# Performance work log

Measured on AMD Instinct MI355X. Metric: run time of the kernel, lower is better.

The kernel has to match this reference:

```python
import jax, jax.numpy as jnp
import numpy as np

# ---- static config (matches init_kwargs) ----
B, N, DIM = 1, 2048, 1024
H, KVH, D = 16, 8, 64
GQ = H // KVH                 # grouped queries per kv head
WS = 64                       # sliding window size (causal, exact)
CBS, STRIDE = 32, 16          # compress block size / sliding stride
SEL_BLK, NSEL, NMEM = 32, 4, 1
NCB = N // STRIDE             # num compressed blocks (128)
NFB = N // SEL_BLK            # num fine blocks (64)
NCPF = SEL_BLK // STRIDE      # compressed blocks per fine block (2)
HID = CBS * D                 # compress MLP hidden (expand factor 1.0)
SCALE = D ** -0.5
THETA = 10000.0
NEG = -jnp.finfo(jnp.float32).max


def setup_inputs():
    key = jax.random.key(0)
    ks = jax.random.split(key, 16)
    s = 0.02
    r = lambda i, shape: jax.random.normal(ks[i], shape, jnp.float32) * s
    return {
        "inp": jax.random.normal(ks[0], (B, N, DIM), jnp.float32),
        "norm_g": jnp.ones((DIM,), jnp.float32),
        "Wqkv": r(1, (DIM, (H + 2 * KVH) * D)),
        "mem_kv": r(2, (2, KVH, NMEM, D)),
        "k_pos": r(3, (KVH, CBS, D)),
        "v_pos": r(4, (KVH, CBS, D)),
        "kW1": r(5, (CBS * D, HID)), "kb1": jnp.zeros((HID,), jnp.float32),
        "kW2": r(6, (HID, D)), "kb2": jnp.zeros((D,), jnp.float32),
        "vW1": r(7, (CBS * D, HID)), "vb1": jnp.zeros((HID,), jnp.float32),
        "vW2": r(8, (HID, D)), "vb2": jnp.zeros((D,), jnp.float32),
        "combW": r(9, (DIM, 3 * H)),
        "combB": jnp.tile(jnp.array([-2.0, -2.0, 2.0], jnp.float32), H),
        "Wout": r(10, (H * D, DIM)),
    }


def _rope(t):
    # lucidrains rotary-embedding-torch: interleaved adjacent-pair rotation
    inv_freq = 1.0 / (THETA ** (jnp.arange(0, D, 2, dtype=jnp.float32) / D))
    ang = jnp.arange(N, dtype=jnp.float32)[:, None] * inv_freq        # [N, D/2]
    cos = jnp.repeat(jnp.cos(ang), 2, axis=-1)                        # [N, D]
    sin = jnp.repeat(jnp.sin(ang), 2, axis=-1)
    t2 = t.reshape(*t.shape[:-1], D // 2, 2)
    rot = jnp.stack([-t2[..., 1], t2[..., 0]], axis=-1).reshape(t.shape)
    return t * cos + rot * sin


def _forward(inp, norm_g, Wqkv, mem_kv, k_pos, v_pos,
             kW1, kb1, kW2, kb2, vW1, vb1, vW2, vb2,
             combW, combB, Wout):
    # RMSNorm
    x = inp * jax.lax.rsqrt(jnp.mean(inp * inp, -1, keepdims=True)
                            + jnp.finfo(inp.dtype).eps) * norm_g
    qkv = x @ Wqkv
    q, k, v = jnp.split(qkv, [H * D, H * D + KVH * D], axis=-1)
    q = q.reshape(B, N, H, D).transpose(0, 2, 1, 3)      # b h n d
    k = k.reshape(B, N, KVH, D).transpose(0, 2, 1, 3)    # b kvh n d
    v = v.reshape(B, N, KVH, D).transpose(0, 2, 1, 3)

    # ---- compressed branch (overlapping windows, left zero pad) ----
    overlap = CBS - STRIDE
    kp = jnp.pad(k, ((0, 0), (0, 0), (overlap, 0), (0, 0)))
    vp = jnp.pad(v, ((0, 0), (0, 0), (overlap, 0), (0, 0)))
    widx = jnp.arange(NCB)[:, None] * STRIDE + jnp.arange(CBS)[None, :]  # [NCB, CBS]
    kw = kp[:, :, widx] + k_pos[None, :, None]   # b kvh w cbs d
    vw = vp[:, :, widx] + v_pos[None, :, None]

    def cmlp(t, W1, b1, W2, b2):
        t = t.reshape(B, KVH, NCB, CBS * D)
        return jax.nn.relu(t @ W1 + b1) @ W2 + b2       # b kvh w d

    ck = cmlp(kw, kW1, kb1, kW2, kb2)
    cv = cmlp(vw, vW1, vb1, vW2, vb2)
    ck = jnp.concatenate([jnp.broadcast_to(mem_kv[0], (B, KVH, NMEM, D)), ck], 2)
    cv = jnp.concatenate([jnp.broadcast_to(mem_kv[1], (B, KVH, NMEM, D)), cv], 2)

    qg = q.reshape(B, KVH, GQ, N, D)
    csim = jnp.einsum('bhgid,bhjd->bhgij', qg, ck) * SCALE   # no mask (cmask=None)
    cattn = jax.nn.softmax(csim, -1)
    cout = jnp.einsum('bhgij,bhjd->bhgid', cattn, cv).reshape(B, H, N, D)

    # rotary AFTER compressed attention (as in source)
    rq, rk = _rope(q), _rope(k)

    # ---- importance scores -> top-k fine block selection ----
    imp = csim[..., NMEM:].mean(2)                          # b kvh n NCB (share grouped q)
    imp = imp.reshape(B, KVH, N, NFB, NCPF).mean(-1)        # mean-pool to fine blocks
    q_blk = jnp.arange(N) // SEL_BLK
    diag = q_blk[:, None] == jnp.arange(NFB)[None, :]
    imp = jnp.where(diag[None, None], NEG, imp)             # mask own (diagonal) block
    imp = jax.nn.softmax(jnp.pad(imp, ((0, 0),) * 3 + ((1, 0),),
                                 constant_values=-1000.0), -1)[..., 1:]
    sel_val, sel_idx = jax.lax.top_k(imp, NSEL)             # b kvh n NSEL

    # ---- fine (block-selected) attention ----
    own = jnp.broadcast_to(q_blk[None, None, :, None], (B, KVH, N, 1))
    sel_idx = jnp.concatenate([sel_idx, own], -1)           # append own block
    fmask = jnp.repeat((sel_val > 1e-10)[..., None], SEL_BLK, -1)  # b kvh n NSEL blk
    causal_row = jnp.tril(jnp.ones((SEL_BLK, SEL_BLK), bool))[jnp.arange(N) % SEL_BLK]
    causal = jnp.broadcast_to(causal_row[None, None, :, None, :],
                              (B, KVH, N, 1, SEL_BLK))
    fmask = jnp.concatenate([fmask, causal], 3).reshape(B, KVH, N, (NSEL + 1) * SEL_BLK)

    fk_blocks = rk.reshape(B, KVH, NFB, SEL_BLK, D)
    fv_blocks = v.reshape(B, KVH, NFB, SEL_BLK, D)
    gather = jax.vmap(jax.vmap(lambda blocks, idx: blocks[idx]))  # over b, kvh
    fk = gather(fk_blocks, sel_idx).reshape(B, KVH, N, (NSEL + 1) * SEL_BLK, D)
    fv = gather(fv_blocks, sel_idx).reshape(B, KVH, N, (NSEL + 1) * SEL_BLK, D)

    rqg = rq.reshape(B, KVH, GQ, N, D)
    fsim = jnp.einsum('bhgid,bhijd->bhgij', rqg, fk) * SCALE
    fsim = jnp.where(fmask[:, :, None], fsim, NEG / 10)
    fattn = jax.nn.softmax(fsim, -1)
    fout = jnp.einsum('bhgij,bhijd->bhgid', fattn, fv).reshape(B, H, N, D)

    # ---- sliding window (causal, exact window size WS) ----
    NW = N // WS
    kp2 = jnp.pad(rk, ((0, 0), (0, 0), (WS, 0), (0, 0)))
    vp2 = jnp.pad(v, ((0, 0), (0, 0), (WS, 0), (0, 0)))
    kidx = jnp.arange(NW)[:, None] * WS + jnp.arange(2 * WS)[None, :]
    kwin = kp2[:, :, kidx]                                  # b kvh nw 2ws d
    vwin = vp2[:, :, kidx]
    qwin = rqg.reshape(B, KVH, GQ, NW, WS, D)
    ssim = jnp.einsum('bhgwid,bhwjd->bhgwij', qwin, kwin) * SCALE
    i = jnp.arange(WS)[:, None]
    j = jnp.arange(2 * WS)[None, :]
    diff = i - (j - WS)
    local_ok = (diff >= 0) & (diff < WS)                    # [WS, 2WS]
    keypos = jnp.arange(NW)[:, None, None] * WS + (jnp.arange(2 * WS) - WS)[None, None, :]
    smask = local_ok[None] & (keypos >= 0)                  # [NW, WS, 2WS]
    ssim = jnp.where(smask[None, None, None], ssim, NEG)
    sattn = jax.nn.softmax(ssim, -1)
    sout = jnp.einsum('bhgwij,bhwjd->bhgwid', sattn, vwin).reshape(B, H, N, D)

    # ---- learned strategy combination (compressed, fine, sliding) ----
    gates = jax.nn.sigmoid(x @ combW + combB).reshape(B, N, H, 3).transpose(0, 2, 1, 3)
    out = gates[..., 0:1] * cout + gates[..., 1:2] * fout + gates[..., 2:3] * sout
    out = out.transpose(0, 2, 1, 3).reshape(B, N, H * D) @ Wout
    return out


def reference(inp, norm_g, Wqkv, mem_kv, k_pos, v_pos,
              kW1, kb1, kW2, kb2, vW1, vb1, vW2, vb2,
              combW, combB, Wout):
    return _forward(inp, norm_g, Wqkv, mem_kv, k_pos, v_pos,
                    kW1, kb1, kW2, kb2, vW1, vb1, vW2, vb2,
                    combW, combB, Wout)
```

## Files before the change

kernel.cpp:

```cpp
#include <hip/hip_runtime.h>
#include <hip/hip_bf16.h>

#define NTOK 2048
#define DIM 1024
#define NH 16
#define KVH 8
#define GQ 2
#define HD 64
#define WS 64
#define CBS 32
#define STRIDE 16
#define SEL_BLK 32
#define NSEL 4
#define NMEM 1
#define NCB 128
#define NFB 64
#define HIDN 2048
#define SCALE 0.125f
#define NEGF (-3.4028234663852886e38f)
#define NEG10F (-3.4028234663852886e37f)

typedef __attribute__((ext_vector_type(8))) short bf16x8;
typedef __attribute__((ext_vector_type(4))) float f32x4;

__device__ __forceinline__ float bflo(unsigned u) { return __uint_as_float(u << 16); }
__device__ __forceinline__ float bfhi(unsigned u) { return __uint_as_float(u & 0xffff0000u); }
__device__ __forceinline__ void dot8(const float4& qa, const float4& qb, uint4 a, float& s) {
    s += qa.x * bflo(a.x) + qa.y * bfhi(a.x) + qa.z * bflo(a.y) + qa.w * bfhi(a.y) +
         qb.x * bflo(a.z) + qb.y * bfhi(a.z) + qb.z * bflo(a.w) + qb.w * bfhi(a.w);
}

__device__ __forceinline__ void gload_lds16(const void* g, void* l) {
    __builtin_amdgcn_global_load_lds((const __attribute__((address_space(1))) unsigned*)g,
                                     (__attribute__((address_space(3))) unsigned*)l, 16, 0, 0);
}

__global__ __launch_bounds__(256) void rmsnorm_kernel(const float* __restrict__ inp,
                                                      const float* __restrict__ g,
                                                      float* __restrict__ x,
                                                      __hip_bfloat16* __restrict__ xb) {
    int n = blockIdx.x;
    const float* row = inp + (size_t)n * DIM;
    float ss = 0.f;
    for (int c = threadIdx.x; c < DIM; c += 256) { float v = row[c]; ss += v * v; }
    __shared__ float red[4];
    for (int o = 32; o; o >>= 1) ss += __shfl_down(ss, o, 64);
    if ((threadIdx.x & 63) == 0) red[threadIdx.x >> 6] = ss;
    __syncthreads();
    if (threadIdx.x == 0) red[0] = red[0] + red[1] + red[2] + red[3];
    __syncthreads();
    float rs = 1.0f / sqrtf(red[0] / (float)DIM + 1.1920928955078125e-07f);
    float* xr = x + (size_t)n * DIM;
    __hip_bfloat16* xbr = xb + (size_t)n * DIM;
    for (int c = threadIdx.x; c < DIM; c += 256) {
        float v = row[c] * rs * g[c];
        xr[c] = v;
        xbr[c] = __float2bfloat16(v);
    }
}

__device__ __forceinline__ void transpose_body(const float* __restrict__ B,
                                               __hip_bfloat16* __restrict__ Bt,
                                               int K, int N, int bx, int by) {
    __shared__ float tile[32][33];
    int n0 = bx * 32, k0 = by * 32;
    int x = threadIdx.x & 31, y = threadIdx.x >> 5;
    for (int i = 0; i < 4; i++) {
        int k = k0 + y + 8 * i, n = n0 + x;
        tile[y + 8 * i][x] = (k < K && n < N) ? B[(size_t)k * N + n] : 0.f;
    }
    __syncthreads();
    for (int i = 0; i < 4; i++) {
        int n = n0 + y + 8 * i, k = k0 + x;
        if (n < N && k < K) Bt[(size_t)n * K + k] = __float2bfloat16(tile[x][y + 8 * i]);
    }
}

__global__ __launch_bounds__(256) void transpose_all_kernel(
    const float* Wqkv, __hip_bfloat16* Wqkvt,
    const float* kW1, __hip_bfloat16* kW1t,
    const float* vW1, __hip_bfloat16* vW1t,
    const float* Wout, __hip_bfloat16* Woutt,
    const float* combW, __hip_bfloat16* combWt,
    const float* kW2, __hip_bfloat16* kW2t,
    const float* vW2, __hip_bfloat16* vW2t) {
    int b = blockIdx.x;
    if (b < 2048) { transpose_body(Wqkv, Wqkvt, 1024, 2048, b % 64, b / 64); return; }
    b -= 2048;
    if (b < 4096) { transpose_body(kW1, kW1t, 2048, 2048, b % 64, b / 64); return; }
    b -= 4096;
    if (b < 4096) { transpose_body(vW1, vW1t, 2048, 2048, b % 64, b / 64); return; }
    b -= 4096;
    if (b < 1024) { transpose_body(Wout, Woutt, 1024, 1024, b % 32, b / 32); return; }
    b -= 1024;
    if (b < 64) { transpose_body(combW, combWt, 1024, 48, b % 2, b / 2); return; }
    b -= 64;
    if (b < 128) { transpose_body(kW2, kW2t, 2048, 64, b % 2, b / 2); return; }
    b -= 128;
    transpose_body(vW2, vW2t, 2048, 64, b % 2, b / 2);
}

template <int ACT, int OUTBF16>
__device__ __forceinline__ void mfma_gemm_body(const __hip_bfloat16* __restrict__ A,
                                               const __hip_bfloat16* __restrict__ Bt,
                                               const float* __restrict__ bias,
                                               void* __restrict__ Cp,
                                               int M, int N, int K, int bx, int by) {
    __shared__ __align__(16) short As[128 * 32];
    __shared__ __align__(16) short Bs[128 * 32];
    int tid = threadIdx.x;
    int lane = tid & 63, wave = tid >> 6;
    int wm = (wave >> 1) * 64, wn = (wave & 1) * 64;
    int m0 = by * 128, n0 = bx * 128;
    f32x4 acc[4][4];
    for (int r = 0; r < 4; r++)
        for (int c = 0; c < 4; c++)
            acc[r][c] = (f32x4){0.f, 0.f, 0.f, 0.f};

    int r0 = tid >> 2, kc0 = (tid & 3) * 8;
    int r1 = r0 + 64;

    for (int k0 = 0; k0 < K; k0 += 32) {
        __syncthreads();
        gload_lds16(A + (size_t)(m0 + r0) * K + k0 + kc0, &As[r0 * 32 + kc0]);
        gload_lds16(A + (size_t)(m0 + r1) * K + k0 + kc0, &As[r1 * 32 + kc0]);
        gload_lds16(Bt + (size_t)(n0 + r0) * K + k0 + kc0, &Bs[r0 * 32 + kc0]);
        gload_lds16(Bt + (size_t)(n0 + r1) * K + k0 + kc0, &Bs[r1 * 32 + kc0]);
        __syncthreads();
        bf16x8 af[4], bfr[4];
#pragma unroll
        for (int r = 0; r < 4; r++)
            af[r] = *(const bf16x8*)&As[(wm + r * 16 + (lane & 15)) * 32 + (lane >> 4) * 8];
#pragma unroll
// ... 19 lines not shown
                else
                    ((float*)Cp)[(size_t)(grow + v) * N + gcol] = val;
            }
        }
    }
}

template <int ACT, int OUTBF16>
__global__ __launch_bounds__(256) void mfma_gemm(const __hip_bfloat16* __restrict__ A,
                                                 const __hip_bfloat16* __restrict__ Bt,
                                                 const float* __restrict__ bias,
                                                 void* __restrict__ Cp,
                                                 int M, int N, int K) {
    mfma_gemm_body<ACT, OUTBF16>(A, Bt, bias, Cp, M, N, K, blockIdx.x, blockIdx.y);
}

__global__ __launch_bounds__(256) void mfma_gemm_pair(const __hip_bfloat16* A0,
                                                      const __hip_bfloat16* A1,
                                                      const __hip_bfloat16* Bt0,
                                                      const __hip_bfloat16* Bt1,
                                                      const float* bias0, const float* bias1,
                                                      __hip_bfloat16* C0, __hip_bfloat16* C1,
                                                      int M, int N, int K) {
    if (blockIdx.z == 0)
        mfma_gemm_body<1, 1>(A0, Bt0, bias0, C0, M, N, K, blockIdx.x, blockIdx.y);
    else
        mfma_gemm_body<1, 1>(A1, Bt1, bias1, C1, M, N, K, blockIdx.x, blockIdx.y);
}

__device__ __forceinline__ void skgemm_body(const __hip_bfloat16* __restrict__ A,
                                            const __hip_bfloat16* __restrict__ Bt,
                                            float* __restrict__ C,
                                            int M, int Nout, int K, int by, int bz, int nz) {
    __shared__ __align__(16) short As[128 * 32];
    __shared__ __align__(16) short Bs[64 * 32];
    int tid = threadIdx.x;
    int lane = tid & 63, wave = tid >> 6;
    int m0 = by * 128;
    int wm = wave * 32;
    int kchunk = K / nz;
    int kbase = bz * kchunk;
    f32x4 acc[2][4];
    for (int r = 0; r < 2; r++)
        for (int c = 0; c < 4; c++) acc[r][c] = (f32x4){0.f, 0.f, 0.f, 0.f};

    int ra = tid >> 2, kc = (tid & 3) * 8;
    int rb = ra < Nout ? ra : Nout - 1;
    for (int k0 = kbase; k0 < kbase + kchunk; k0 += 32) {
        __syncthreads();
        gload_lds16(A + (size_t)(m0 + ra) * K + k0 + kc, &As[ra * 32 + kc]);
        gload_lds16(A + (size_t)(m0 + ra + 64) * K + k0 + kc, &As[(ra + 64) * 32 + kc]);
        gload_lds16(Bt + (size_t)rb * K + k0 + kc, &Bs[ra * 32 + kc]);
        __syncthreads();
        bf16x8 af[2], bfr[4];
#pragma unroll
        for (int r = 0; r < 2; r++)
            af[r] = *(const bf16x8*)&As[(wm + r * 16 + (lane & 15)) * 32 + (lane >> 4) * 8];
#pragma unroll
        for (int c = 0; c < 4; c++)
            bfr[c] = *(const bf16x8*)&Bs[(c * 16 + (lane & 15)) * 32 + (lane >> 4) * 8];
#pragma unroll
        for (int r = 0; r < 2; r++)
#pragma unroll
            for (int c = 0; c < 4; c++)
                acc[r][c] = __builtin_amdgcn_mfma_f32_16x16x32_bf16(af[r], bfr[c], acc[r][c], 0, 0, 0);
    }
    for (int r = 0; r < 2; r++) {
        int grow = m0 + wm + r * 16 + (lane >> 4) * 4;
        for (int c = 0; c < 4; c++) {
            int gcol = c * 16 + (lane & 15);
            if (gcol >= Nout) continue;
#pragma unroll
            for (int v = 0; v < 4; v++)
                atomicAdd(&C[(size_t)(grow + v) * Nout + gcol], acc[r][c][v]);
        }
    }
}

__global__ __launch_bounds__(256) void skgemm_kernel(const __hip_bfloat16* __restrict__ A,
                                                     const __hip_bfloat16* __restrict__ Bt,
                                                     float* __restrict__ C,
                                                     int M, int Nout, int K) {
    skgemm_body(A, Bt, C, M, Nout, K, blockIdx.y, blockIdx.z, gridDim.z);
}

__global__ __launch_bounds__(256) void skgemm_pair(const __hip_bfloat16* A0,
                                                   const __hip_bfloat16* A1,
                                                   const __hip_bfloat16* Bt0,
                                                   const __hip_bfloat16* Bt1,
                                                   float* C0, float* C1,
                                                   int M, int Nout, int K) {
    if (blockIdx.x == 0)
        skgemm_body(A0, Bt0, C0, M, Nout, K, blockIdx.y, blockIdx.z, gridDim.z);
    else
        skgemm_body(A1, Bt1, C1, M, Nout, K, blockIdx.y, blockIdx.z, gridDim.z);
}

__global__ __launch_bounds__(256) void initbias2_kernel(float* __restrict__ C0,
                                                        const float* __restrict__ b0,
                                                        float* __restrict__ C1,
                                                        const float* __restrict__ b1,
                                                        int M, int Nout) {
    int idx = blockIdx.x * 256 + threadIdx.x;
    int tot = M * Nout;
    if (idx < tot) C0[idx] = b0[idx % Nout];
    else if (idx < 2 * tot) { idx -= tot; C1[idx] = b1[idx % Nout]; }
}

__global__ __launch_bounds__(256) void initbias_kernel(float* __restrict__ C,
                                                       const float* __restrict__ bias,
                                                       int M, int Nout) {
    int idx = blockIdx.x * 256 + threadIdx.x;
    if (idx < M * Nout) C[idx] = bias[idx % Nout];
}

__global__ __launch_bounds__(256) void buildwin_kernel(const float* __restrict__ qkv,
                                                       const float* __restrict__ k_pos,
                                                       const float* __restrict__ v_pos,
                                                       __hip_bfloat16* __restrict__ kwflat,
                                                       __hip_bfloat16* __restrict__ vwflat) {
    size_t total = (size_t)(KVH * NCB) * HIDN;
    for (size_t e = (size_t)blockIdx.x * 256 + threadIdx.x; e < total;
         e += (size_t)gridDim.x * 256) {
        int r = (int)(e >> 11);
        int c = (int)(e & 2047);
        int j = c >> 6, d = c & 63;
        int h = r >> 7, i = r & 127;
        int p = i * STRIDE + j - (CBS - STRIDE);
        float kb = k_pos[((size_t)h * CBS + j) * HD + d];
        float vb = v_pos[((size_t)h * CBS + j) * HD + d];
        float kv = 0.f, vv = 0.f;
        if (p >= 0) {
            kv = qkv[(size_t)p * 2048 + 1024 + h * HD + d];
            vv = qkv[(size_t)p * 2048 + 1536 + h * HD + d];
        }
        kwflat[e] = __float2bfloat16(kv + kb);
        vwflat[e] = __float2bfloat16(vv + vb);
    }
}

__global__ __launch_bounds__(256) void rope_kernel(const float* __restrict__ qkv,
                                                   float* __restrict__ rq,
                                                   __hip_bfloat16* __restrict__ rk,
                                                   __hip_bfloat16* __restrict__ vt) {
    int n = blockIdx.x;
    int t = threadIdx.x;
    for (int idx = t; idx < NH * 32; idx += 256) {
        int h = idx >> 5, f = idx & 31;
        float inv = exp2f((float)f * -0.41524101186092f);
        float ang = (float)n * inv;
        float cc = cosf(ang), ssn = sinf(ang);
        float a = qkv[(size_t)n * 2048 + h * HD + 2 * f];
        float b = qkv[(size_t)n * 2048 + h * HD + 2 * f + 1];
        float* o = rq + ((size_t)h * NTOK + n) * HD + 2 * f;
        o[0] = a * cc - b * ssn;
        o[1] = b * cc + a * ssn;
    }
    for (int idx = t; idx < KVH * 32; idx += 256) {
        int h = idx >> 5, f = idx & 31;
        float inv = exp2f((float)f * -0.41524101186092f);
        float ang = (float)n * inv;
        float cc = cosf(ang), ssn = sinf(ang);
        float a = qkv[(size_t)n * 2048 + 1024 + h * HD + 2 * f];
        float b = qkv[(size_t)n * 2048 + 1024 + h * HD + 2 * f + 1];
        __hip_bfloat16* o = rk + ((size_t)h * NTOK + n) * HD + 2 * f;
        o[0] = __float2bfloat16(a * cc - b * ssn);
        o[1] = __float2bfloat16(b * cc + a * ssn);
    }
    for (int idx = t; idx < KVH * HD; idx += 256) {
        int h = idx >> 6, d = idx & 63;
        vt[((size_t)h * NTOK + n) * HD + d] =
            __float2bfloat16(qkv[(size_t)n * 2048 + 1536 + h * HD + d]);
    }
}

__global__ __launch_bounds__(256) void cattn2_kernel(const float* __restrict__ qkv,
                                                     const float* __restrict__ ckraw,
                                                     const float* __restrict__ cvraw,
                                                     const float* __restrict__ memkv,
                                                     float* __restrict__ cout,
                                                     int* __restrict__ selidx,
                                                     int* __restrict__ selmask) {
    int h = blockIdx.x >> 6;
    int i0 = (blockIdx.x & 63) * 32;
    int t = threadIdx.x;
    __shared__ float qs[64][68];
    __shared__ float sc[64][132];
    __shared__ float scratch[32 * 68];
    __shared__ float memk[64], memv[64];

    for (int idx = t; idx < 4096; idx += 256) {
        int row = idx >> 6, d = idx & 63;
        int g = row >> 5, qi = row & 31;
        qs[row][d] = qkv[(size_t)(i0 + qi) * 2048 + (h * 2 + g) * 64 + d];
    }
    if (t < 64) { memk[t] = memkv[h * 64 + t]; memv[t] = memkv[(8 + h) * 64 + t]; }
    __syncthreads();
    if (t < 64) {
        float s = 0.f;
        for (int d = 0; d < 64; d++) s += qs[t][d] * memk[d];
// ... 76 lines not shown
            o1[dd] = p1 * v;
        }
    }
    for (int c = 0; c < 4; c++) {
        __syncthreads();
        for (int idx = t; idx < 2048; idx += 256) {
            int jj = idx >> 6, d = idx & 63;
            scratch[jj * 68 + d] = cvraw[((size_t)h * 128 + c * 32 + jj) * 64 + d];
        }
        __syncthreads();
        for (int jj = 0; jj < 32; jj++) {
            float p0 = sc[rg * 2][1 + c * 32 + jj];
            float p1 = sc[rg * 2 + 1][1 + c * 32 + jj];
#pragma unroll
            for (int dd = 0; dd < 8; dd++) {
                float v = scratch[jj * 68 + dg + dd * 8];
                o0[dd] += p0 * v;
                o1[dd] += p1 * v;
            }
        }
    }
    {
        int row = rg * 2;
        int g = row >> 5, qi = row & 31;
        int g2 = (row + 1) >> 5, qi2 = (row + 1) & 31;
#pragma unroll
        for (int dd = 0; dd < 8; dd++) {
            cout[(((size_t)(h * 2 + g)) * NTOK + i0 + qi) * 64 + dd * 8 + dg] = o0[dd];
            cout[(((size_t)(h * 2 + g2)) * NTOK + i0 + qi2) * 64 + dd * 8 + dg] = o1[dd];
        }
    }
}

__global__ __launch_bounds__(256) void attn_fused_kernel(const float* __restrict__ rq,
                                                         const __hip_bfloat16* __restrict__ rk,
                                                         const __hip_bfloat16* __restrict__ vt,
                                                         const int* __restrict__ selidx,
                                                         const int* __restrict__ selmask,
                                                         float* __restrict__ fout,
                                                         float* __restrict__ sout) {
    int ws = threadIdx.x >> 6, lane = threadIdx.x & 63;
    __shared__ float sp[4][2][160];
    __shared__ int sel[4][5];
    __shared__ int smk[4];
    float* p0 = sp[ws][0];
    float* p1 = sp[ws][1];

    int kq = lane >> 2, c = lane & 3;
    int kv8 = lane >> 3, c8 = lane & 7;

    if (blockIdx.x < 4096) {
        int wid = blockIdx.x * 4 + ws;
        int h = wid >> 11, i = wid & 2047;
        if (lane < 5) sel[ws][lane] = selidx[((size_t)h * NTOK + i) * 5 + lane];
        if (lane == 5) smk[ws] = selmask[h * NTOK + i];

        const float* q0p = rq + ((size_t)(h * 2 + 0) * NTOK + i) * 64 + c * 16;
        const float* q1p = rq + ((size_t)(h * 2 + 1) * NTOK + i) * 64 + c * 16;
        float4 q0[4], q1[4];
#pragma unroll
        for (int u = 0; u < 4; u++) {
            q0[u] = *(const float4*)(q0p + u * 4);
            q1[u] = *(const float4*)(q1p + u * 4);
        }
        __syncthreads();
        int mk = smk[ws];
        int iq = i & 31;
#pragma unroll
        for (int kt = 0; kt < 10; kt++) {
            int slot = kt >> 1;
            int blk = sel[ws][slot];
            int key = kt * 16 + kq;
            int jj = key & 31;
            int kpos = blk * 32 + jj;
            bool valid = (slot < 4) ? (((mk >> slot) & 1) != 0) : (jj <= iq);
            const __hip_bfloat16* kr = rk + ((size_t)h * NTOK + kpos) * 64 + c * 16;
            float s0 = 0.f, s1 = 0.f;
            uint4 a = *(const uint4*)(kr);
            uint4 b = *(const uint4*)(kr + 8);
            dot8(q0[0], q0[1], a, s0); dot8(q0[2], q0[3], b, s0);
            dot8(q1[0], q1[1], a, s1); dot8(q1[2], q1[3], b, s1);
            s0 += __shfl_xor(s0, 1); s0 += __shfl_xor(s0, 2);
            s1 += __shfl_xor(s1, 1); s1 += __shfl_xor(s1, 2);
            if (c == 0) {
                p0[key] = valid ? s0 * SCALE : NEG10F;
// ... 33 lines not shown
        for (int slot = 0; slot < 5; slot++) {
            const __hip_bfloat16* vbase = vt + ((size_t)h * NTOK + sel[ws][slot] * 32) * 64;
#pragma unroll
            for (int pass = 0; pass < 4; pass++) {
                int j = pass * 8 + kv8;
                uint4 v = *(const uint4*)(vbase + j * 64 + c8 * 8);
                float pa = p0[slot * 32 + j], pb = p1[slot * 32 + j];
                float e0 = bflo(v.x), e1 = bfhi(v.x), e2 = bflo(v.y), e3 = bfhi(v.y);
                float e4 = bflo(v.z), e5 = bfhi(v.z), e6 = bflo(v.w), e7 = bfhi(v.w);
                o0[0] = fmaf(pa, e0, o0[0]); o0[1] = fmaf(pa, e1, o0[1]);
                o0[2] = fmaf(pa, e2, o0[2]); o0[3] = fmaf(pa, e3, o0[3]);
                o0[4] = fmaf(pa, e4, o0[4]); o0[5] = fmaf(pa, e5, o0[5]);
                o0[6] = fmaf(pa, e6, o0[6]); o0[7] = fmaf(pa, e7, o0[7]);
                o1[0] = fmaf(pb, e0, o1[0]); o1[1] = fmaf(pb, e1, o1[1]);
                o1[2] = fmaf(pb, e2, o1[2]); o1[3] = fmaf(pb, e3, o1[3]);
                o1[4] = fmaf(pb, e4, o1[4]); o1[5] = fmaf(pb, e5, o1[5]);
                o1[6] = fmaf(pb, e6, o1[6]); o1[7] = fmaf(pb, e7, o1[7]);
            }
        }
#pragma unroll
        for (int o = 8; o <= 32; o <<= 1)
#pragma unroll
            for (int d = 0; d < 8; d++) {
                o0[d] += __shfl_xor(o0[d], o);
                o1[d] += __shfl_xor(o1[d], o);
            }
        if (kv8 == 0) {
            float* f0 = fout + ((size_t)(h * 2 + 0) * NTOK + i) * 64 + c8 * 8;
            float* f1 = fout + ((size_t)(h * 2 + 1) * NTOK + i) * 64 + c8 * 8;
            *(float4*)(f0) = (float4){o0[0], o0[1], o0[2], o0[3]};
            *(float4*)(f0 + 4) = (float4){o0[4], o0[5], o0[6], o0[7]};
            *(float4*)(f1) = (float4){o1[0], o1[1], o1[2], o1[3]};
            *(float4*)(f1 + 4) = (float4){o1[4], o1[5], o1[6], o1[7]};
        }
    } else {
        int wid = (blockIdx.x - 4096) * 4 + ws;
        int h = wid >> 11, i = wid & 2047;
        const float* q0p = rq + ((size_t)(h * 2 + 0) * NTOK + i) * 64 + c * 16;
        const float* q1p = rq + ((size_t)(h * 2 + 1) * NTOK + i) * 64 + c * 16;
        float4 q0[4], q1[4];
#pragma unroll
        for (int u = 0; u < 4; u++) {
            q0[u] = *(const float4*)(q0p + u * 4);
            q1[u] = *(const float4*)(q1p + u * 4);
        }
#pragma unroll
        for (int kt = 0; kt < 4; kt++) {
            int key = kt * 16 + kq;
            int kpos = i - 63 + key;
            int kp = kpos < 0 ? 0 : kpos;
            const __hip_bfloat16* kr = rk + ((size_t)h * NTOK + kp) * 64 + c * 16;
            float s0 = 0.f, s1 = 0.f;
            uint4 a = *(const uint4*)(kr);
            uint4 b = *(const uint4*)(kr + 8);
            dot8(q0[0], q0[1], a, s0); dot8(q0[2], q0[3], b, s0);
            dot8(q1[0], q1[1], a, s1); dot8(q1[2], q1[3], b, s1);
            s0 += __shfl_xor(s0, 1); s0 += __shfl_xor(s0, 2);
            s1 += __shfl_xor(s1, 1); s1 += __shfl_xor(s1, 2);
            if (c == 0) {
                p0[key] = (kpos >= 0) ? s0 * SCALE : NEG10F;
                p1[key] = (kpos >= 0) ? s1 * SCALE : NEG10F;
            }
        }
        __syncthreads();
        {
            float a0 = p0[lane], a1 = p1[lane];
            float m0 = a0, m1 = a1;
#pragma unroll
            for (int o = 1; o < 64; o <<= 1) {
                m0 = fmaxf(m0, __shfl_xor(m0, o));
                m1 = fmaxf(m1, __shfl_xor(m1, o));
            }
            float e0 = __expf(a0 - m0), e1 = __expf(a1 - m1);
            float d0 = e0, d1 = e1;
#pragma unroll
            for (int o = 1; o < 64; o <<= 1) {
                d0 += __shfl_xor(d0, o);
                d1 += __shfl_xor(d1, o);
            }
            p0[lane] = e0 / d0;
            p1[lane] = e1 / d1;
        }
        __syncthreads();
        int base = i - 63;
        float o0[8] = {}, o1[8] = {};
        const __hip_bfloat16* vbase = vt + (size_t)h * NTOK * 64;
#pragma unroll
        for (int pass = 0; pass < 8; pass++) {
            int j = pass * 8 + kv8;
            int kpos = base + j;
            int kp = kpos < 0 ? 0 : kpos;
            uint4 v = *(const uint4*)(vbase + (size_t)kp * 64 + c8 * 8);
            float pa = p0[j], pb = p1[j];
            float e0 = bflo(v.x), e1 = bfhi(v.x), e2 = bflo(v.y), e3 = bfhi(v.y);
            float e4 = bflo(v.z), e5 = bfhi(v.z), e6 = bflo(v.w), e7 = bfhi(v.w);
            o0[0] = fmaf(pa, e0, o0[0]); o0[1] = fmaf(pa, e1, o0[1]);
            o0[2] = fmaf(pa, e2, o0[2]); o0[3] = fmaf(pa, e3, o0[3]);
            o0[4] = fmaf(pa, e4, o0[4]); o0[5] = fmaf(pa, e5, o0[5]);
            o0[6] = fmaf(pa, e6, o0[6]); o0[7] = fmaf(pa, e7, o0[7]);
            o1[0] = fmaf(pb, e0, o1[0]); o1[1] = fmaf(pb, e1, o1[1]);
            o1[2] = fmaf(pb, e2, o1[2]); o1[3] = fmaf(pb, e3, o1[3]);
            o1[4] = fmaf(pb, e4, o1[4]); o1[5] = fmaf(pb, e5, o1[5]);
            o1[6] = fmaf(pb, e6, o1[6]); o1[7] = fmaf(pb, e7, o1[7]);
        }
#pragma unroll
        for (int o = 8; o <= 32; o <<= 1)
#pragma unroll
            for (int d = 0; d < 8; d++) {
                o0[d] += __shfl_xor(o0[d], o);
                o1[d] += __shfl_xor(o1[d], o);
            }
        if (kv8 == 0) {
            float* s0p = sout + ((size_t)(h * 2 + 0) * NTOK + i) * 64 + c8 * 8;
            float* s1p = sout + ((size_t)(h * 2 + 1) * NTOK + i) * 64 + c8 * 8;
            *(float4*)(s0p) = (float4){o0[0], o0[1], o0[2], o0[3]};
            *(float4*)(s0p + 4) = (float4){o0[4], o0[5], o0[6], o0[7]};
            *(float4*)(s1p) = (float4){o1[0], o1[1], o1[2], o1[3]};
            *(float4*)(s1p + 4) = (float4){o1[4], o1[5], o1[6], o1[7]};
        }
    }
}

__global__ __launch_bounds__(256) void combine_kernel(const float* __restrict__ gateslin,
                                                      const float* __restrict__ cout,
                                                      const float* __restrict__ fout,
                                                      const float* __restrict__ sout,
                                                      __hip_bfloat16* __restrict__ att) {
    int n = blockIdx.x;
    for (int c = threadIdx.x; c < NH * HD; c += 256) {
        int hd = c >> 6, d = c & 63;
        float g0 = 1.f / (1.f + expf(-gateslin[(size_t)n * (NH * 3) + hd * 3 + 0]));
        float g1 = 1.f / (1.f + expf(-gateslin[(size_t)n * (NH * 3) + hd * 3 + 1]));
        float g2 = 1.f / (1.f + expf(-gateslin[(size_t)n * (NH * 3) + hd * 3 + 2]));
        size_t o = ((size_t)hd * NTOK + n) * HD + d;
        att[(size_t)n * (NH * HD) + c] =
            __float2bfloat16(g0 * cout[o] + g1 * fout[o] + g2 * sout[o]);
    }
}

extern "C" void kernel_launch(void* const* d_in, const int* in_sizes, int n_in,
                              void* d_out, int out_size, void* d_ws, size_t ws_size,
                              hipStream_t stream) {
    const float* inp    = (const float*)d_in[0];
    const float* norm_g = (const float*)d_in[1];
    const float* Wqkv   = (const float*)d_in[2];
    const float* mem_kv = (const float*)d_in[3];
    const float* k_pos  = (const float*)d_in[4];
    const float* v_pos  = (const float*)d_in[5];
    const float* kW1    = (const float*)d_in[6];
    const float* kb1    = (const float*)d_in[7];
    const float* kW2    = (const float*)d_in[8];
// ... 12 lines not shown
    auto alloc = [&](size_t bytes) {
        void* p = base + off;
        off += (bytes + 255) & ~(size_t)255;
        return p;
    };
    float* x            = (float*)alloc((size_t)NTOK * DIM * 4);
    __hip_bfloat16* xb  = (__hip_bfloat16*)alloc((size_t)NTOK * DIM * 2);
    float* qkv          = (float*)alloc((size_t)NTOK * 2048 * 4);
    __hip_bfloat16* Wqkvt = (__hip_bfloat16*)alloc((size_t)2048 * 1024 * 2);
    __hip_bfloat16* kW1t  = (__hip_bfloat16*)alloc((size_t)2048 * 2048 * 2);
    __hip_bfloat16* vW1t  = (__hip_bfloat16*)alloc((size_t)2048 * 2048 * 2);
    __hip_bfloat16* Woutt = (__hip_bfloat16*)alloc((size_t)1024 * 1024 * 2);
    __hip_bfloat16* combWt = (__hip_bfloat16*)alloc((size_t)48 * 1024 * 2);
    __hip_bfloat16* kW2t  = (__hip_bfloat16*)alloc((size_t)64 * 2048 * 2);
    __hip_bfloat16* vW2t  = (__hip_bfloat16*)alloc((size_t)64 * 2048 * 2);
    __hip_bfloat16* kwflat = (__hip_bfloat16*)alloc((size_t)KVH * NCB * HIDN * 2);
    __hip_bfloat16* vwflat = (__hip_bfloat16*)alloc((size_t)KVH * NCB * HIDN * 2);
    __hip_bfloat16* hidkb = (__hip_bfloat16*)alloc((size_t)KVH * NCB * HIDN * 2);
    __hip_bfloat16* hidvb = (__hip_bfloat16*)alloc((size_t)KVH * NCB * HIDN * 2);
    float* ckraw        = (float*)alloc((size_t)KVH * NCB * HD * 4);
    float* cvraw        = (float*)alloc((size_t)KVH * NCB * HD * 4);
    float* rq           = (float*)alloc((size_t)NH * NTOK * HD * 4);
    __hip_bfloat16* rk  = (__hip_bfloat16*)alloc((size_t)KVH * NTOK * HD * 2);
    __hip_bfloat16* vt  = (__hip_bfloat16*)alloc((size_t)KVH * NTOK * HD * 2);
    float* coutb        = (float*)alloc((size_t)NH * NTOK * HD * 4);
    float* foutb        = (float*)alloc((size_t)NH * NTOK * HD * 4);
    float* soutb        = (float*)alloc((size_t)NH * NTOK * HD * 4);
    float* gatesb       = (float*)alloc((size_t)NTOK * NH * 3 * 4);
    __hip_bfloat16* attb = (__hip_bfloat16*)alloc((size_t)NTOK * DIM * 2);
    int* selidx         = (int*)alloc((size_t)KVH * NTOK * 5 * 4);
    int* selmask        = (int*)alloc((size_t)KVH * NTOK * 4);
    (void)ws_size; (void)in_sizes; (void)n_in; (void)out_size;

    rmsnorm_kernel<<<NTOK, 256, 0, stream>>>(inp, norm_g, x, xb);
    transpose_all_kernel<<<11584, 256, 0, stream>>>(Wqkv, Wqkvt, kW1, kW1t, vW1, vW1t,
                                                    Wout, Woutt, combW, combWt,
                                                    kW2, kW2t, vW2, vW2t);
    mfma_gemm<0, 0><<<dim3(16, 16), 256, 0, stream>>>(xb, Wqkvt, nullptr, qkv, 2048, 2048, 1024);
    initbias_kernel<<<(NTOK * 48 + 255) / 256, 256, 0, stream>>>(gatesb, combB, NTOK, 48);
    skgemm_kernel<<<dim3(1, 16, 4), 256, 0, stream>>>(xb, combWt, gatesb, 2048, 48, 1024);
    buildwin_kernel<<<4096, 256, 0, stream>>>(qkv, k_pos, v_pos, kwflat, vwflat);
    mfma_gemm_pair<<<dim3(16, 8, 2), 256, 0, stream>>>(kwflat, vwflat, kW1t, vW1t,
                                                       kb1, vb1, hidkb, hidvb,
                                                       1024, 2048, 2048);
    initbias2_kernel<<<(2 * 1024 * 64 + 255) / 256, 256, 0, stream>>>(ckraw, kb2, cvraw, vb2, 1024, 64);
    skgemm_pair<<<dim3(2, 8, 8), 256, 0, stream>>>(hidkb, hidvb, kW2t, vW2t,
                                                   ckraw, cvraw, 1024, 64, 2048);
    rope_kernel<<<NTOK, 256, 0, stream>>>(qkv, rq, rk, vt);
    cattn2_kernel<<<KVH * (NTOK / 32), 256, 0, stream>>>(qkv, ckraw, cvraw, mem_kv,
                                                         coutb, selidx, selmask);
    attn_fused_kernel<<<8192, 256, 0, stream>>>(rq, rk, vt, selidx, selmask, foutb, soutb);
    combine_kernel<<<NTOK, 256, 0, stream>>>(gatesb, coutb, foutb, soutb, attb);
    mfma_gemm<0, 0><<<dim3(8, 16), 256, 0, stream>>>(attb, Woutt, nullptr, out, 2048, 1024, 1024);
}
```

Measured before the change: 411.8 us.

## Merge preprocessing launches and tile sliding-window attention through LDS

Folds RMSNorm, the weight transposes and the bias initialisations into one pre-kernel. It also merges the QKV GEMM with the gate GEMM, and the window-building step with RoPE, so several small launches become fewer larger ones. The sliding-window attention branch now stages a 127-row K/V window per 64-query tile in padded LDS and reuses it across 16 queries per wave, instead of each wave reading keys and values from global memory per query. This cuts launch overhead and global traffic. The cost is larger, more divergent kernels and higher LDS use, which can lower occupancy.

```diff
diff --git a/kernel.cpp b/kernel.cpp
--- a/kernel.cpp
+++ b/kernel.cpp
@@ -35,11 +35,10 @@
                                      (__attribute__((address_space(3))) unsigned*)l, 16, 0, 0);
 }
 
-__global__ __launch_bounds__(256) void rmsnorm_kernel(const float* __restrict__ inp,
-                                                      const float* __restrict__ g,
-                                                      float* __restrict__ x,
-                                                      __hip_bfloat16* __restrict__ xb) {
-    int n = blockIdx.x;
+__device__ __forceinline__ void rms_body(const float* __restrict__ inp,
+                                         const float* __restrict__ g,
+                                         float* __restrict__ x,
+                                         __hip_bfloat16* __restrict__ xb, int n) {
     const float* row = inp + (size_t)n * DIM;
     float ss = 0.f;
     for (int c = threadIdx.x; c < DIM; c += 256) { float v = row[c]; ss += v * v; }
@@ -76,15 +75,21 @@
     }
 }
 
-__global__ __launch_bounds__(256) void transpose_all_kernel(
+__global__ __launch_bounds__(256) void pre_kernel(
+    const float* inp, const float* norm_g, float* x, __hip_bfloat16* xb,
     const float* Wqkv, __hip_bfloat16* Wqkvt,
     const float* kW1, __hip_bfloat16* kW1t,
     const float* vW1, __hip_bfloat16* vW1t,
     const float* Wout, __hip_bfloat16* Woutt,
     const float* combW, __hip_bfloat16* combWt,
     const float* kW2, __hip_bfloat16* kW2t,
-    const float* vW2, __hip_bfloat16* vW2t) {
+    const float* vW2, __hip_bfloat16* vW2t,
+    const float* combB, float* gatesb,
+    const float* kb2, float* ckraw,
+    const float* vb2, float* cvraw) {
     int b = blockIdx.x;
+    if (b < 2048) { rms_body(inp, norm_g, x, xb, b); return; }
+    b -= 2048;
     if (b < 2048) { transpose_body(Wqkv, Wqkvt, 1024, 2048, b % 64, b / 64); return; }
     b -= 2048;
     if (b < 4096) { transpose_body(kW1, kW1t, 2048, 2048, b % 64, b / 64); return; }
@@ -97,8 +102,23 @@
     b -= 64;
     if (b < 128) { transpose_body(kW2, kW2t, 2048, 64, b % 2, b / 2); return; }
     b -= 128;
-    transpose_body(vW2, vW2t, 2048, 64, b % 2, b / 2);
-}
+    if (b < 128) { transpose_body(vW2, vW2t, 2048, 64, b % 2, b / 2); return; }
+    b -= 128;
+    if (b < 384) {
+        int idx = b * 256 + threadIdx.x;
+        if (idx < 2048 * 48) gatesb[idx] = combB[idx % 48];
+        return;
+    }
+    b -= 384;
+    {
+        int idx = b * 256 + threadIdx.x;
+        int tot = 1024 * 64;
+        if (idx < tot) ckraw[idx] = kb2[idx % 64];
+        else if (idx < 2 * tot) { idx -= tot; cvraw[idx] = vb2[idx % 64]; }
+        return;
+    }
+}
+#define PRE_BLOCKS (2048 + 2048 + 4096 + 4096 + 1024 + 64 + 128 + 128 + 384 + 512)
 
 template <int ACT, int OUTBF16>
 __device__ __forceinline__ void mfma_gemm_body(const __hip_bfloat16* __restrict__ A,
@@ -184,8 +204,8 @@
                                             const __hip_bfloat16* __restrict__ Bt,
                                             float* __restrict__ C,
                                             int M, int Nout, int K, int by, int bz, int nz) {
-    __shared__ __align__(16) short As[128 * 32];
-    __shared__ __align__(16) short Bs[64 * 32];
+    __shared__ __align__(16) short As2[128 * 32];
+    __shared__ __align__(16) short Bs2[64 * 32];
     int tid = threadIdx.x;
     int lane = tid & 63, wave = tid >> 6;
     int m0 = by * 128;
@@ -200,17 +220,17 @@
     int rb = ra < Nout ? ra : Nout - 1;
     for (int k0 = kbase; k0 < kbase + kchunk; k0 += 32) {
         __syncthreads();
-        gload_lds16(A + (size_t)(m0 + ra) * K + k0 + kc, &As[ra * 32 + kc]);
-        gload_lds16(A + (size_t)(m0 + ra + 64) * K + k0 + kc, &As[(ra + 64) * 32 + kc]);
-        gload_lds16(Bt + (size_t)rb * K + k0 + kc, &Bs[ra * 32 + kc]);
+        gload_lds16(A + (size_t)(m0 + ra) * K + k0 + kc, &As2[ra * 32 + kc]);
+        gload_lds16(A + (size_t)(m0 + ra + 64) * K + k0 + kc, &As2[(ra + 64) * 32 + kc]);
+        gload_lds16(Bt + (size_t)rb * K + k0 + kc, &Bs2[ra * 32 + kc]);
         __syncthreads();
         bf16x8 af[2], bfr[4];
 #pragma unroll
         for (int r = 0; r < 2; r++)
-            af[r] = *(const bf16x8*)&As[(wm + r * 16 + (lane & 15)) * 32 + (lane >> 4) * 8];
+            af[r] = *(const bf16x8*)&As2[(wm + r * 16 + (lane & 15)) * 32 + (lane >> 4) * 8];
 #pragma unroll
         for (int c = 0; c < 4; c++)
-            bfr[c] = *(const bf16x8*)&Bs[(c * 16 + (lane & 15)) * 32 + (lane >> 4) * 8];
+            bfr[c] = *(const bf16x8*)&Bs2[(c * 16 + (lane & 15)) * 32 + (lane >> 4) * 8];
 #pragma unroll
         for (int r = 0; r < 2; r++)
 #pragma unroll
@@ -229,11 +249,18 @@
     }
 }
 
-__global__ __launch_bounds__(256) void skgemm_kernel(const __hip_bfloat16* __restrict__ A,
-                                                     const __hip_bfloat16* __restrict__ Bt,
-                                                     float* __restrict__ C,
-                                                     int M, int Nout, int K) {
-    skgemm_body(A, Bt, C, M, Nout, K, blockIdx.y, blockIdx.z, gridDim.z);
+__global__ __launch_bounds__(256) void qkv_gates_kernel(const __hip_bfloat16* xb,
+                                                        const __hip_bfloat16* Wqkvt,
+                                                        float* qkv,
+                                                        const __hip_bfloat16* combWt,
+                                                        float* gatesb) {
+    int b = blockIdx.x;
+    if (b < 256) {
+        mfma_gemm_body<0, 0>(xb, Wqkvt, nullptr, qkv, 2048, 2048, 1024, b & 15, b >> 4);
+    } else {
+        int s = b - 256;
+        skgemm_body(xb, combWt, gatesb, 2048, 48, 1024, s & 15, s >> 4, 4);
+    }
 }
 
 __global__ __launch_bounds__(256) void skgemm_pair(const __hip_bfloat16* A0,
@@ -248,65 +275,47 @@
         skgemm_body(A1, Bt1, C1, M, Nout, K, blockIdx.y, blockIdx.z, gridDim.z);
 }
 
-__global__ __launch_bounds__(256) void initbias2_kernel(float* __restrict__ C0,
-                                                        const float* __restrict__ b0,
-                                                        float* __restrict__ C1,
-                                                        const float* __restrict__ b1,
-                                                        int M, int Nout) {
-    int idx = blockIdx.x * 256 + threadIdx.x;
-    int tot = M * Nout;
-    if (idx < tot) C0[idx] = b0[idx % Nout];
-    else if (idx < 2 * tot) { idx -= tot; C1[idx] = b1[idx % Nout]; }
-}
-
-__global__ __launch_bounds__(256) void initbias_kernel(float* __restrict__ C,
-                                                       const float* __restrict__ bias,
-                                                       int M, int Nout) {
-    int idx = blockIdx.x * 256 + threadIdx.x;
-    if (idx < M * Nout) C[idx] = bias[idx % Nout];
-}
-
-__global__ __launch_bounds__(256) void buildwin_kernel(const float* __restrict__ qkv,
-                                                       const float* __restrict__ k_pos,
-                                                       const float* __restrict__ v_pos,
-                                                       __hip_bfloat16* __restrict__ kwflat,
-                                                       __hip_bfloat16* __restrict__ vwflat) {
-    size_t total = (size_t)(KVH * NCB) * HIDN;
-    for (size_t e = (size_t)blockIdx.x * 256 + threadIdx.x; e < total;
-         e += (size_t)gridDim.x * 256) {
-        int r = (int)(e >> 11);
-        int c = (int)(e & 2047);
-        int j = c >> 6, d = c & 63;
-        int h = r >> 7, i = r & 127;
-        int p = i * STRIDE + j - (CBS - STRIDE);
-        float kb = k_pos[((size_t)h * CBS + j) * HD + d];
-        float vb = v_pos[((size_t)h * CBS + j) * HD + d];
-        float kv = 0.f, vv = 0.f;
-        if (p >= 0) {
-            kv = qkv[(size_t)p * 2048 + 1024 + h * HD + d];
-            vv = qkv[(size_t)p * 2048 + 1536 + h * HD + d];
-        }
-        kwflat[e] = __float2bfloat16(kv + kb);
-        vwflat[e] = __float2bfloat16(vv + vb);
-    }
-}
-
-__global__ __launch_bounds__(256) void rope_kernel(const float* __restrict__ qkv,
-                                                   float* __restrict__ rq,
-                                                   __hip_bfloat16* __restrict__ rk,
-                                                   __hip_bfloat16* __restrict__ vt) {
-    int n = blockIdx.x;
+__global__ __launch_bounds__(256) void winrope_kernel(const float* __restrict__ qkv,
+                                                      const float* __restrict__ k_pos,
+                                                      const float* __restrict__ v_pos,
+                                                      __hip_bfloat16* __restrict__ kwflat,
+                                                      __hip_bfloat16* __restrict__ vwflat,
+                                                      float* __restrict__ rq,
+                                                      __hip_bfloat16* __restrict__ rk,
+                                                      __hip_bfloat16* __restrict__ vt) {
+    int b = blockIdx.x;
     int t = threadIdx.x;
+    if (b < 4096) {
+        size_t total = (size_t)(KVH * NCB) * HIDN;
+        for (size_t e = (size_t)b * 256 + t; e < total; e += (size_t)4096 * 256) {
+            int r = (int)(e >> 11);
+            int c = (int)(e & 2047);
+            int j = c >> 6, d = c & 63;
+            int h = r >> 7, i = r & 127;
+            int p = i * STRIDE + j - (CBS - STRIDE);
+            float kb = k_pos[((size_t)h * CBS + j) * HD + d];
+            float vb = v_pos[((size_t)h * CBS + j) * HD + d];
+            float kv = 0.f, vv = 0.f;
+            if (p >= 0) {
+                kv = qkv[(size_t)p * 2048 + 1024 + h * HD + d];
+                vv = qkv[(size_t)p * 2048 + 1536 + h * HD + d];
+            }
+            kwflat[e] = __float2bfloat16(kv + kb);
+            vwflat[e] = __float2bfloat16(vv + vb);
+        }
+        return;
+    }
+    int n = b - 4096;
     for (int idx = t; idx < NH * 32; idx += 256) {
         int h = idx >> 5, f = idx & 31;
         float inv = exp2f((float)f * -0.41524101186092f);
         float ang = (float)n * inv;
         float cc = cosf(ang), ssn = sinf(ang);
         float a = qkv[(size_t)n * 2048 + h * HD + 2 * f];
-        float b = qkv[(size_t)n * 2048 + h * HD + 2 * f + 1];
+        float bq = qkv[(size_t)n * 2048 + h * HD + 2 * f + 1];
         float* o = rq + ((size_t)h * NTOK + n) * HD + 2 * f;
-        o[0] = a * cc - b * ssn;
-        o[1] = b * cc + a * ssn;
+        o[0] = a * cc - bq * ssn;
+        o[1] = bq * cc + a * ssn;
     }
     for (int idx = t; idx < KVH * 32; idx += 256) {
         int h = idx >> 5, f = idx & 31;
@@ -314,10 +323,10 @@
         float ang = (float)n * inv;
         float cc = cosf(ang), ssn = sinf(ang);
         float a = qkv[(size_t)n * 2048 + 1024 + h * HD + 2 * f];
-        float b = qkv[(size_t)n * 2048 + 1024 + h * HD + 2 * f + 1];
+        float bq = qkv[(size_t)n * 2048 + 1024 + h * HD + 2 * f + 1];
         __hip_bfloat16* o = rk + ((size_t)h * NTOK + n) * HD + 2 * f;
-        o[0] = __float2bfloat16(a * cc - b * ssn);
-        o[1] = __float2bfloat16(b * cc + a * ssn);
+        o[0] = __float2bfloat16(a * cc - bq * ssn);
+        o[1] = __float2bfloat16(bq * cc + a * ssn);
     }
     for (int idx = t; idx < KVH * HD; idx += 256) {
         int h = idx >> 6, d = idx & 63;
@@ -460,25 +469,129 @@
     }
 }
 
-__global__ __launch_bounds__(256) void attn_fused_kernel(const float* __restrict__ rq,
-                                                         const __hip_bfloat16* __restrict__ rk,
-                                                         const __hip_bfloat16* __restrict__ vt,
-                                                         const int* __restrict__ selidx,
-                                                         const int* __restrict__ selmask,
-                                                         float* __restrict__ fout,
-                                                         float* __restrict__ sout) {
-    int ws = threadIdx.x >> 6, lane = threadIdx.x & 63;
-    __shared__ float sp[4][2][160];
+#define SWROWPAD 72
+__global__ __launch_bounds__(256) void attn_fused2_kernel(const float* __restrict__ rq,
+                                                          const __hip_bfloat16* __restrict__ rk,
+                                                          const __hip_bfloat16* __restrict__ vt,
+                                                          const int* __restrict__ selidx,
+                                                          const int* __restrict__ selmask,
+                                                          float* __restrict__ fout,
+                                                          float* __restrict__ sout) {
+    int tid = threadIdx.x;
+    int ws = tid >> 6, lane = tid & 63;
+    __shared__ __align__(16) char smem[2 * 128 * SWROWPAD * 2 + 4 * 128 * 4];
     __shared__ int sel[4][5];
     __shared__ int smk[4];
-    float* p0 = sp[ws][0];
-    float* p1 = sp[ws][1];
 
     int kq = lane >> 2, c = lane & 3;
     int kv8 = lane >> 3, c8 = lane & 7;
 
-    if (blockIdx.x < 4096) {
-        int wid = blockIdx.x * 4 + ws;
+    if (blockIdx.x < 256) {
+        int h = blockIdx.x >> 5;
+        int q0 = (blockIdx.x & 31) * 64;
+        short* ks = (short*)smem;
+        short* vs = ks + 128 * SWROWPAD;
+        float* ps = (float*)(vs + 128 * SWROWPAD);
+        int basek = q0 - 63;
+        for (int idx = tid; idx < 127 * 8; idx += 256) {
+            int row = idx >> 3, ch = (idx & 7) * 8;
+            int kpos = basek + row;
+            uint4 kv = (uint4){0u, 0u, 0u, 0u}, vv = (uint4){0u, 0u, 0u, 0u};
+            if (kpos >= 0) {
+                kv = *(const uint4*)(rk + ((size_t)h * NTOK + kpos) * 64 + ch);
+                vv = *(const uint4*)(vt + ((size_t)h * NTOK + kpos) * 64 + ch);
+            }
+            *(uint4*)&ks[row * SWROWPAD + ch] = kv;
+            *(uint4*)&vs[row * SWROWPAD + ch] = vv;
+        }
+        __syncthreads();
+        float* p0 = ps + ws * 128;
+        float* p1 = p0 + 64;
+#pragma unroll 1
+        for (int tq = 0; tq < 16; tq++) {
+            int i = q0 + ws * 16 + tq;
+            int ibase = ws * 16 + tq;
+            const float* q0p = rq + ((size_t)(h * 2 + 0) * NTOK + i) * 64 + c * 16;
+            const float* q1p = rq + ((size_t)(h * 2 + 1) * NTOK + i) * 64 + c * 16;
+            float4 qa[4], qb[4];
+#pragma unroll
+            for (int u = 0; u < 4; u++) {
+                qa[u] = *(const float4*)(q0p + u * 4);
+                qb[u] = *(const float4*)(q1p + u * 4);
+            }
+#pragma unroll
+            for (int kt = 0; kt < 4; kt++) {
+                int key = kt * 16 + kq;
+                const short* kr = &ks[(ibase + key) * SWROWPAD + c * 16];
+                float s0 = 0.f, s1 = 0.f;
+                uint4 a = *(const uint4*)(kr);
+                uint4 b = *(const uint4*)(kr + 8);
+                dot8(qa[0], qa[1], a, s0); dot8(qa[2], qa[3], b, s0);
+                dot8(qb[0], qb[1], a, s1); dot8(qb[2], qb[3], b, s1);
+                s0 += __shfl_xor(s0, 1); s0 += __shfl_xor(s0, 2);
+                s1 += __shfl_xor(s1, 1); s1 += __shfl_xor(s1, 2);
+                int kpos = i - 63 + key;
+                if (c == 0) {
+                    p0[key] = (kpos >= 0) ? s0 * SCALE : NEG10F;
+                    p1[key] = (kpos >= 0) ? s1 * SCALE : NEG10F;
+                }
+            }
+            {
+                float a0 = p0[lane], a1 = p1[lane];
+                float m0 = a0, m1 = a1;
+#pragma unroll
+                for (int o = 1; o < 64; o <<= 1) {
+                    m0 = fmaxf(m0, __shfl_xor(m0, o));
+                    m1 = fmaxf(m1, __shfl_xor(m1, o));
+                }
+                float e0 = __expf(a0 - m0), e1 = __expf(a1 - m1);
+                float d0 = e0, d1 = e1;
+#pragma unroll
+                for (int o = 1; o < 64; o <<= 1) {
+                    d0 += __shfl_xor(d0, o);
+                    d1 += __shfl_xor(d1, o);
+                }
+                p0[lane] = e0 / d0;
+                p1[lane] = e1 / d1;
+            }
+            float o0[8] = {}, o1[8] = {};
+#pragma unroll
+            for (int pass = 0; pass < 8; pass++) {
+                int j = pass * 8 + kv8;
+                uint4 v = *(const uint4*)&vs[(ibase + j) * SWROWPAD + c8 * 8];
+                float pa = p0[j], pb = p1[j];
+                float e0 = bflo(v.x), e1 = bfhi(v.x), e2 = bflo(v.y), e3 = bfhi(v.y);
+                float e4 = bflo(v.z), e5 = bfhi(v.z), e6 = bflo(v.w), e7 = bfhi(v.w);
+                o0[0] = fmaf(pa, e0, o0[0]); o0[1] = fmaf(pa, e1, o0[1]);
+                o0[2] = fmaf(pa, e2, o0[2]); o0[3] = fmaf(pa, e3, o0[3]);
+                o0[4] = fmaf(pa, e4, o0[4]); o0[5] = fmaf(pa, e5, o0[5]);
+                o0[6] = fmaf(pa, e6, o0[6]); o0[7] = fmaf(pa, e7, o0[7]);
+                o1[0] = fmaf(pb, e0, o1[0]); o1[1] = fmaf(pb, e1, o1[1]);
+                o1[2] = fmaf(pb, e2, o1[2]); o1[3] = fmaf(pb, e3, o1[3]);
+                o1[4] = fmaf(pb, e4, o1[4]); o1[5] = fmaf(pb, e5, o1[5]);
+                o1[6] = fmaf(pb, e6, o1[6]); o1[7] = fmaf(pb, e7, o1[7]);
+            }
+#pragma unroll
+            for (int o = 8; o <= 32; o <<= 1)
+#pragma unroll
+                for (int d = 0; d < 8; d++) {
+                    o0[d] += __shfl_xor(o0[d], o);
+                    o1[d] += __shfl_xor(o1[d], o);
+                }
+            if (kv8 == 0) {
+                float* s0p = sout + ((size_t)(h * 2 + 0) * NTOK + i) * 64 + c8 * 8;
+                float* s1p = sout + ((size_t)(h * 2 + 1) * NTOK + i) * 64 + c8 * 8;
+                *(float4*)(s0p) = (float4){o0[0], o0[1], o0[2], o0[3]};
+                *(float4*)(s0p + 4) = (float4){o0[4], o0[5], o0[6], o0[7]};
+                *(float4*)(s1p) = (float4){o1[0], o1[1], o1[2], o1[3]};
+                *(float4*)(s1p + 4) = (float4){o1[4], o1[5], o1[6], o1[7]};
+            }
+        }
+    } else {
+        float* spbase = (float*)smem;
+        float* p0 = spbase + ws * 320;
+        float* p1 = p0 + 160;
+        int wid = (blockIdx.x - 256) * 4 + ws;
         int h = wid >> 11, i = wid & 2047;
         if (lane < 5) sel[ws][lane] = selidx[((size_t)h * NTOK + i) * 5 + lane];
         if (lane == 5) smk[ws] = selmask[h * NTOK + i];
@@ -578,91 +691,6 @@
             *(float4*)(f0 + 4) = (float4){o0[4], o0[5], o0[6], o0[7]};
             *(float4*)(f1) = (float4){o1[0], o1[1], o1[2], o1[3]};
             *(float4*)(f1 + 4) = (float4){o1[4], o1[5], o1[6], o1[7]};
-        }
-    } else {
-        int wid = (blockIdx.x - 4096) * 4 + ws;
-        int h = wid >> 11, i = wid & 2047;
-        const float* q0p = rq + ((size_t)(h * 2 + 0) * NTOK + i) * 64 + c * 16;
-        const float* q1p = rq + ((size_t)(h * 2 + 1) * NTOK + i) * 64 + c * 16;
-        float4 q0[4], q1[4];
-#pragma unroll
-        for (int u = 0; u < 4; u++) {
-            q0[u] = *(const float4*)(q0p + u * 4);
-            q1[u] = *(const float4*)(q1p + u * 4);
-        }
-#pragma unroll
-        for (int kt = 0; kt < 4; kt++) {
-            int key = kt * 16 + kq;
-            int kpos = i - 63 + key;
-            int kp = kpos < 0 ? 0 : kpos;
-            const __hip_bfloat16* kr = rk + ((size_t)h * NTOK + kp) * 64 + c * 16;
-            float s0 = 0.f, s1 = 0.f;
-            uint4 a = *(const uint4*)(kr);
-            uint4 b = *(const uint4*)(kr + 8);
-            dot8(q0[0], q0[1], a, s0); dot8(q0[2], q0[3], b, s0);
-            dot8(q1[0], q1[1], a, s1); dot8(q1[2], q1[3], b, s1);
-            s0 += __shfl_xor(s0, 1); s0 += __shfl_xor(s0, 2);
-            s1 += __shfl_xor(s1, 1); s1 += __shfl_xor(s1, 2);
-            if (c == 0) {
-                p0[key] = (kpos >= 0) ? s0 * SCALE : NEG10F;
-                p1[key] = (kpos >= 0) ? s1 * SCALE : NEG10F;
-            }
-        }
-        __syncthreads();
-        {
-            float a0 = p0[lane], a1 = p1[lane];
-            float m0 = a0, m1 = a1;
-#pragma unroll
-            for (int o = 1; o < 64; o <<= 1) {
-                m0 = fmaxf(m0, __shfl_xor(m0, o));
-                m1 = fmaxf(m1, __shfl_xor(m1, o));
-            }
-            float e0 = __expf(a0 - m0), e1 = __expf(a1 - m1);
-            float d0 = e0, d1 = e1;
-#pragma unroll
-            for (int o = 1; o < 64; o <<= 1) {
-                d0 += __shfl_xor(d0, o);
-                d1 += __shfl_xor(d1, o);
-            }
-            p0[lane] = e0 / d0;
-            p1[lane] = e1 / d1;
-        }
-        __syncthreads();
-        int base = i - 63;
-        float o0[8] = {}, o1[8] = {};
-        const __hip_bfloat16* vbase = vt + (size_t)h * NTOK * 64;
-#pragma unroll
-        for (int pass = 0; pass < 8; pass++) {
-            int j = pass * 8 + kv8;
-            int kpos = base + j;
-            int kp = kpos < 0 ? 0 : kpos;
-            uint4 v = *(const uint4*)(vbase + (size_t)kp * 64 + c8 * 8);
-            float pa = p0[j], pb = p1[j];
-            float e0 = bflo(v.x), e1 = bfhi(v.x), e2 = bflo(v.y), e3 = bfhi(v.y);
-            float e4 = bflo(v.z), e5 = bfhi(v.z), e6 = bflo(v.w), e7 = bfhi(v.w);
-            o0[0] = fmaf(pa, e0, o0[0]); o0[1] = fmaf(pa, e1, o0[1]);
-            o0[2] = fmaf(pa, e2, o0[2]); o0[3] = fmaf(pa, e3, o0[3]);
-            o0[4] = fmaf(pa, e4, o0[4]); o0[5] = fmaf(pa, e5, o0[5]);
-            o0[6] = fmaf(pa, e6, o0[6]); o0[7] = fmaf(pa, e7, o0[7]);
-            o1[0] = fmaf(pb, e0, o1[0]); o1[1] = fmaf(pb, e1, o1[1]);
-            o1[2] = fmaf(pb, e2, o1[2]); o1[3] = fmaf(pb, e3, o1[3]);
-            o1[4] = fmaf(pb, e4, o1[4]); o1[5] = fmaf(pb, e5, o1[5]);
-            o1[6] = fmaf(pb, e6, o1[6]); o1[7] = fmaf(pb, e7, o1[7]);
-        }
-#pragma unroll
-        for (int o = 8; o <= 32; o <<= 1)
-#pragma unroll
-            for (int d = 0; d < 8; d++) {
-                o0[d] += __shfl_xor(o0[d], o);
-                o1[d] += __shfl_xor(o1[d], o);
-            }
-        if (kv8 == 0) {
-            float* s0p = sout + ((size_t)(h * 2 + 0) * NTOK + i) * 64 + c8 * 8;
-            float* s1p = sout + ((size_t)(h * 2 + 1) * NTOK + i) * 64 + c8 * 8;
-            *(float4*)(s0p) = (float4){o0[0], o0[1], o0[2], o0[3]};
-            *(float4*)(s0p + 4) = (float4){o0[4], o0[5], o0[6], o0[7]};
-            *(float4*)(s1p) = (float4){o1[0], o1[1], o1[2], o1[3]};
-            *(float4*)(s1p + 4) = (float4){o1[4], o1[5], o1[6], o1[7]};
         }
     }
 }
@@ -741,24 +769,23 @@
     int* selmask        = (int*)alloc((size_t)KVH * NTOK * 4);
     (void)ws_size; (void)in_sizes; (void)n_in; (void)out_size;
 
-    rmsnorm_kernel<<<NTOK, 256, 0, stream>>>(inp, norm_g, x, xb);
-    transpose_all_kernel<<<11584, 256, 0, stream>>>(Wqkv, Wqkvt, kW1, kW1t, vW1, vW1t,
-                                                    Wout, Woutt, combW, combWt,
-                                                    kW2, kW2t, vW2, vW2t);
-    mfma_gemm<0, 0><<<dim3(16, 16), 256, 0, stream>>>(xb, Wqkvt, nullptr, qkv, 2048, 2048, 1024);
-    initbias_kernel<<<(NTOK * 48 + 255) / 256, 256, 0, stream>>>(gatesb, combB, NTOK, 48);
-    skgemm_kernel<<<dim3(1, 16, 4), 256, 0, stream>>>(xb, combWt, gatesb, 2048, 48, 1024);
-    buildwin_kernel<<<4096, 256, 0, stream>>>(qkv, k_pos, v_pos, kwflat, vwflat);
+    pre_kernel<<<PRE_BLOCKS, 256, 0, stream>>>(inp, norm_g, x, xb,
+                                               Wqkv, Wqkvt, kW1, kW1t, vW1, vW1t,
+                                               Wout, Woutt, combW, combWt,
+                                               kW2, kW2t, vW2, vW2t,
+                                               combB, gatesb, kb2, ckraw, vb2, cvraw);
+    qkv_gates_kernel<<<320, 256, 0, stream>>>(xb, Wqkvt, qkv, combWt, gatesb);
+    winrope_kernel<<<4096 + 2048, 256, 0, stream>>>(qkv, k_pos, v_pos, kwflat, vwflat,
+                                                    rq, rk, vt);
     mfma_gemm_pair<<<dim3(16, 8, 2), 256, 0, stream>>>(kwflat, vwflat, kW1t, vW1t,
                                                        kb1, vb1, hidkb, hidvb,
                                                        1024, 2048, 2048);
-    initbias2_kernel<<<(2 * 1024 * 64 + 255) / 256, 256, 0, stream>>>(ckraw, kb2, cvraw, vb2, 1024, 64);
     skgemm_pair<<<dim3(2, 8, 8), 256, 0, stream>>>(hidkb, hidvb, kW2t, vW2t,
                                                    ckraw, cvraw, 1024, 64, 2048);
-    rope_kernel<<<NTOK, 256, 0, stream>>>(qkv, rq, rk, vt);
     cattn2_kernel<<<KVH * (NTOK / 32), 256, 0, stream>>>(qkv, ckraw, cvraw, mem_kv,
                                                          coutb, selidx, selmask);
-    attn_fused_kernel<<<8192, 256, 0, stream>>>(rq, rk, vt, selidx, selmask, foutb, soutb);
+    attn_fused2_kernel<<<256 + 4096, 256, 0, stream>>>(rq, rk, vt, selidx, selmask,
+                                                       foutb, soutb);
     combine_kernel<<<NTOK, 256, 0, stream>>>(gatesb, coutb, foutb, soutb, attb);
     mfma_gemm<0, 0><<<dim3(8, 16), 256, 0, stream>>>(attb, Woutt, nullptr, out, 2048, 1024, 1024);
 }
```

Result: faster. 379.5 us (-7.8%).
